# Kernel tuning notes

Measured on AMD Instinct MI355X. Metric: run time of the kernel, lower is better.

Reference implementation:

```python
import jax, jax.numpy as jnp
import numpy as np

B, C, V, K, COUT = 4, 64, 40962, 9, 64  # graph_level 6 -> 10*4^6+2 = 40962 vertices


def setup_inputs() -> dict:
    key = jax.random.key(0)
    k1, k2, k3, k4, k5 = jax.random.split(key, 5)
    return {
        "x": jax.random.normal(k1, (B, C, V), dtype=jnp.float32),
        "index": jax.random.randint(k2, (V, K), 0, V),  # per-vertex neighbor ids
        "itp_mat": jax.random.normal(k3, (V, K, K), dtype=jnp.float32) * 0.2,
        "conv_w": jax.random.normal(k4, (COUT, C, 1, K), dtype=jnp.float32) * 0.05,
        "conv_b": jax.random.normal(k5, (COUT,), dtype=jnp.float32) * 0.05,
    }


def reference(x, index, itp_mat, conv_w, conv_b):
    # x: [B, C, V]. Original: permute(2,0,1) -> [V,B,C]; gather neighbors -> [V,K,B,C];
    # select_index = arange(V) (stride=1, select_index=None), so selection is identity.
    g = jnp.transpose(x, (2, 0, 1))[index]          # [V, K, B, C] neighbor gather
    g = jnp.transpose(g, (2, 3, 0, 1))              # [B, C, V, K]
    # Interploate: batched per-vertex matmul [B,C,V,1,K] @ [V,K,K] -> [B,C,V,1,K]
    itp = jnp.einsum('bcvk,vkj->bcvj', g, itp_mat)  # [B, C, V, K]
    # Conv2d with kernel (1, K): contracts C and K per vertex -> [B, COUT, V]
    out = jnp.einsum('bcvj,ocj->bov', itp, conv_w[:, :, 0, :]) + conv_b[None, :, None]
    # sparse_reset: scatter into zeros at select_index = arange(V) -> identity
    return out
```

## Files before the change

### kernel.cpp

```cpp
#include <hip/hip_runtime.h>
#include <hip/hip_bf16.h>

#define VN 40962
#define NG 10241
#define LDA_B 1168
#define LDS_TOT 18688
#define XT_BYTES (VN * 512)

typedef float f32x4 __attribute__((ext_vector_type(4)));
typedef __bf16 bf16x8 __attribute__((ext_vector_type(8)));

__global__ __launch_bounds__(256) void k_transpose(const float* __restrict__ x,
                                                   __bf16* __restrict__ xt) {
    __shared__ __bf16 tile[64][65];
    const int v0 = blockIdx.x * 64;
    const int t0 = blockIdx.y * 64;
    const int lane = threadIdx.x & 63;
    const int sub = threadIdx.x >> 6;

#pragma unroll
    for (int r = 0; r < 16; ++r) {
        const int t = t0 + r * 4 + sub;
        const int v = v0 + lane;
        float val = (v < VN) ? x[(size_t)t * VN + v] : 0.f;
        tile[r * 4 + sub][lane] = (__bf16)val;
    }
    __syncthreads();
#pragma unroll
    for (int r = 0; r < 16; ++r) {
        const int vv = r * 4 + sub;
        const int v = v0 + vv;
        if (v < VN) xt[(size_t)v * 256 + t0 + lane] = tile[lane][vv];
    }
}

__global__ __launch_bounds__(64) void k_wprep(const float* __restrict__ conv_w,
                                              __bf16* __restrict__ wf) {
    const int id = blockIdx.x;
    const int ks = id % 18;
    const int w  = id / 18;
    const int lane = threadIdx.x;
    const int o  = w * 16 + (lane & 15);
    const int kb = (lane >> 4) * 8;
    const float* wrow = conv_w + (size_t)o * 576 + ks * 32 + kb;
    bf16x8 f;
#pragma unroll
    for (int e = 0; e < 8; ++e) f[e] = (__bf16)wrow[e];
    *(bf16x8*)(wf + ((size_t)id * 64 + lane) * 8) = f;
}

__global__ __launch_bounds__(256) void k_fused(const __bf16* __restrict__ xt,
                                               const int* __restrict__ index,
                                               const float* __restrict__ itp_mat,
                                               const __bf16* __restrict__ wf,
                                               const float* __restrict__ conv_b,
                                               float* __restrict__ out) {
    __shared__ char smem[LDS_TOT];

    const int tid  = threadIdx.x;
    const int lane = tid & 63;
    const int w    = tid >> 6;
    const int l16  = lane & 15;
    const int g4   = lane >> 4;

    int g;
    {
        const int bid = blockIdx.x;
        const int xcd = bid & 7;
        const int idx = bid >> 3;
        g = (xcd == 0) ? idx : (1281 + (xcd - 1) * 1280 + idx);
    }
    const int v0 = g * 4;

    float gv[4][9];
#pragma unroll
    for (int vv = 0; vv < 4; ++vv) {
        const int v  = v0 + vv;
        const int vm = (v < VN) ? v : VN - 1;
        const int* idxv = index + (size_t)vm * 9;
#pragma unroll
        for (int k = 0; k < 9; ++k)
            gv[vv][k] = (float)xt[(size_t)idxv[k] * 256 + tid];
    }
#pragma unroll
    for (int vv = 0; vv < 4; ++vv) {
        const int v  = v0 + vv;
        const int vm = (v < VN) ? v : VN - 1;
        const float* am = itp_mat + (size_t)vm * 81;
        float s[9];
#pragma unroll
        for (int j = 0; j < 9; ++j) s[j] = 0.f;
#pragma unroll
        for (int k = 0; k < 9; ++k) {
            const float gk = gv[vv][k];
#pragma unroll
            for (int j = 0; j < 9; ++j) s[j] += gk * am[k * 9 + j];
        }
        __bf16* rowp = (__bf16*)(smem + (vv * 4 + w) * LDA_B) + lane * 9;
#pragma unroll
        for (int j = 0; j < 9; ++j) rowp[j] = (__bf16)s[j];
    }
    __syncthreads();

    f32x4 acc = {0.f, 0.f, 0.f, 0.f};
    {
        const char* ar = smem + l16 * LDA_B + g4 * 16;
        const __bf16* wfp = wf + ((size_t)(w * 18) * 64 + lane) * 8;
#pragma unroll
        for (int ks = 0; ks < 18; ++ks) {
            bf16x8 a  = *(const bf16x8*)(ar + ks * 64);
            bf16x8 wb = *(const bf16x8*)(wfp + (size_t)ks * 512);
            acc = __builtin_amdgcn_mfma_f32_16x16x32_bf16(wb, a, acc, 0, 0, 0);
        }
    }

    {
        const int vvs = l16 >> 2;
        const int bs  = l16 & 3;
        const int v_s = v0 + vvs;
        const int o_b = w * 16 + g4 * 4;
        const f32x4 bias4 = *(const f32x4*)(conv_b + o_b);
        if (v_s < VN) {
            float* ob = out + (size_t)(bs * 64 + o_b) * VN + v_s;
#pragma unroll
            for (int r = 0; r < 4; ++r)
                ob[(size_t)r * VN] = acc[r] + bias4[r];
        }
    }
}

extern "C" void kernel_launch(void* const* d_in, const int* in_sizes, int n_in,
                              void* d_out, int out_size, void* d_ws, size_t ws_size,
                              hipStream_t stream) {
    const float* x       = (const float*)d_in[0];
    const int*   index   = (const int*)d_in[1];
    const float* itp_mat = (const float*)d_in[2];
    const float* conv_w  = (const float*)d_in[3];
    const float* conv_b  = (const float*)d_in[4];
    float* out = (float*)d_out;

    __bf16* xt = (__bf16*)d_ws;
    __bf16* wfrag = (__bf16*)((char*)d_ws + XT_BYTES);

    dim3 tgrid((VN + 63) / 64, 4, 1);
    k_transpose<<<tgrid, 256, 0, stream>>>(x, xt);
    k_wprep<<<72, 64, 0, stream>>>(conv_w, wfrag);
    k_fused<<<NG, 256, 0, stream>>>(xt, index, itp_mat, wfrag, conv_b, out);
}
```

Baseline: 86.82 us.

## Process two vertex groups per block and prefetch the second gather during MFMA

Each block now handles 8 vertices in two halves of 4, halving the grid. The gather for the second half is issued before the first half's MFMA and store, so its global load latency can overlap with compute. __syncthreads is replaced by a raw lgkmcnt wait plus s_barrier, which avoids waiting on outstanding vector memory loads. In exchange it uses more registers for the second gather buffer, which may lower occupancy, and it leaves fewer blocks in flight.

```diff
diff --git a/kernel.cpp b/kernel.cpp
--- a/kernel.cpp
+++ b/kernel.cpp
@@ -2,7 +2,7 @@
 #include <hip/hip_bf16.h>
 
 #define VN 40962
-#define NG 10241
+#define NGB 5121
 #define LDA_B 1168
 #define LDS_TOT 18688
 #define XT_BYTES (VN * 512)
@@ -68,65 +68,90 @@
         const int bid = blockIdx.x;
         const int xcd = bid & 7;
         const int idx = bid >> 3;
-        g = (xcd == 0) ? idx : (1281 + (xcd - 1) * 1280 + idx);
+        g = (xcd == 0) ? idx : (641 + (xcd - 1) * 640 + idx);
     }
-    const int v0 = g * 4;
+    const int v0 = g * 8;
+
+    const int vvs = l16 >> 2;
+    const int bs  = l16 & 3;
+    const int o_b = w * 16 + g4 * 4;
+    const f32x4 bias4 = *(const f32x4*)(conv_b + o_b);
+    float* const ob_base = out + (size_t)(bs * 64 + o_b) * VN;
+
+    const char* ar = smem + l16 * LDA_B + g4 * 16;
+    const __bf16* wfp = wf + ((size_t)(w * 18) * 64 + lane) * 8;
+
+#define INTERP_WRITE(GV, VBASE)                                               \
+    _Pragma("unroll")                                                         \
+    for (int vv = 0; vv < 4; ++vv) {                                          \
+        const int v  = (VBASE) + vv;                                          \
+        const int vm = (v < VN) ? v : VN - 1;                                 \
+        const float* am = itp_mat + (size_t)vm * 81;         \
+        float s[9];                                                           \
+        _Pragma("unroll")                                                     \
+        for (int j = 0; j < 9; ++j) s[j] = 0.f;                               \
+        _Pragma("unroll")                                                     \
+        for (int k = 0; k < 9; ++k) {                                         \
+            const float gk = GV[vv][k];                                       \
+            _Pragma("unroll")                                                 \
+            for (int j = 0; j < 9; ++j) s[j] += gk * am[k * 9 + j];           \
+        }                                                                     \
+        __bf16* rowp = (__bf16*)(smem + (vv * 4 + w) * LDA_B) + lane * 9;     \
+        _Pragma("unroll")                                                     \
+        for (int j = 0; j < 9; ++j) rowp[j] = (__bf16)s[j];                   \
+    }
+
+#define GATHER(GV, VBASE)                                                     \
+    _Pragma("unroll")                                                         \
+    for (int vv = 0; vv < 4; ++vv) {                                          \
+        const int v  = (VBASE) + vv;                                          \
+        const int vm = (v < VN) ? v : VN - 1;                                 \
+        const int* idxv = index + (size_t)vm * 9;                 \
+        _Pragma("unroll")                                                     \
+        for (int k = 0; k < 9; ++k)                                           \
+            GV[vv][k] = (float)xt[(size_t)idxv[k] * 256 + tid];               \
+    }
+
+#define MFMA_STORE(VBASE) {                                                   \
+    f32x4 acc = {0.f, 0.f, 0.f, 0.f};                                         \
+    _Pragma("unroll")                                                         \
+    for (int ks = 0; ks < 18; ++ks) {                                         \
+        bf16x8 a  = *(const bf16x8*)(ar + ks * 64);                           \
+        bf16x8 wb = *(const bf16x8*)(wfp + (size_t)ks * 512);                 \
+        acc = __builtin_amdgcn_mfma_f32_16x16x32_bf16(wb, a, acc, 0, 0, 0);   \
+    }                                                                         \
+    const int v_s = (VBASE) + vvs;                                            \
+    if (v_s < VN) {                                                           \
+        float* ob = ob_base + v_s;                                            \
+        _Pragma("unroll")                                                     \
+        for (int r = 0; r < 4; ++r)                                           \
+            ob[(size_t)r * VN] = acc[r] + bias4[r];                           \
+    } }
+
+#define RAW_BARRIER() do {                                                    \
+        asm volatile("s_waitcnt lgkmcnt(0)" ::: "memory");                    \
+        __builtin_amdgcn_s_barrier();                                         \
+    } while (0)
 
     float gv[4][9];
-#pragma unroll
-    for (int vv = 0; vv < 4; ++vv) {
-        const int v  = v0 + vv;
-        const int vm = (v < VN) ? v : VN - 1;
-        const int* idxv = index + (size_t)vm * 9;
-#pragma unroll
-        for (int k = 0; k < 9; ++k)
-            gv[vv][k] = (float)xt[(size_t)idxv[k] * 256 + tid];
-    }
-#pragma unroll
-    for (int vv = 0; vv < 4; ++vv) {
-        const int v  = v0 + vv;
-        const int vm = (v < VN) ? v : VN - 1;
-        const float* am = itp_mat + (size_t)vm * 81;
-        float s[9];
-#pragma unroll
-        for (int j = 0; j < 9; ++j) s[j] = 0.f;
-#pragma unroll
-        for (int k = 0; k < 9; ++k) {
-            const float gk = gv[vv][k];
-#pragma unroll
-            for (int j = 0; j < 9; ++j) s[j] += gk * am[k * 9 + j];
-        }
-        __bf16* rowp = (__bf16*)(smem + (vv * 4 + w) * LDA_B) + lane * 9;
-#pragma unroll
-        for (int j = 0; j < 9; ++j) rowp[j] = (__bf16)s[j];
-    }
-    __syncthreads();
+    GATHER(gv, v0)
+    INTERP_WRITE(gv, v0)
 
-    f32x4 acc = {0.f, 0.f, 0.f, 0.f};
-    {
-        const char* ar = smem + l16 * LDA_B + g4 * 16;
-        const __bf16* wfp = wf + ((size_t)(w * 18) * 64 + lane) * 8;
-#pragma unroll
-        for (int ks = 0; ks < 18; ++ks) {
-            bf16x8 a  = *(const bf16x8*)(ar + ks * 64);
-            bf16x8 wb = *(const bf16x8*)(wfp + (size_t)ks * 512);
-            acc = __builtin_amdgcn_mfma_f32_16x16x32_bf16(wb, a, acc, 0, 0, 0);
-        }
-    }
+    float gn[4][9];
+    GATHER(gn, v0 + 4)
 
-    {
-        const int vvs = l16 >> 2;
-        const int bs  = l16 & 3;
-        const int v_s = v0 + vvs;
-        const int o_b = w * 16 + g4 * 4;
-        const f32x4 bias4 = *(const f32x4*)(conv_b + o_b);
-        if (v_s < VN) {
-            float* ob = out + (size_t)(bs * 64 + o_b) * VN + v_s;
-#pragma unroll
-            for (int r = 0; r < 4; ++r)
-                ob[(size_t)r * VN] = acc[r] + bias4[r];
-        }
-    }
+    RAW_BARRIER();
+    MFMA_STORE(v0)
+    RAW_BARRIER();
+
+    INTERP_WRITE(gn, v0 + 4)
+    RAW_BARRIER();
+    MFMA_STORE(v0 + 4)
+
+#undef INTERP_WRITE
+#undef GATHER
+#undef MFMA_STORE
+#undef RAW_BARRIER
 }
 
 extern "C" void kernel_launch(void* const* d_in, const int* in_sizes, int n_in,
@@ -145,5 +170,5 @@
     dim3 tgrid((VN + 63) / 64, 4, 1);
     k_transpose<<<tgrid, 256, 0, stream>>>(x, xt);
     k_wprep<<<72, 64, 0, stream>>>(conv_w, wfrag);
-    k_fused<<<NG, 256, 0, stream>>>(xt, index, itp_mat, wfrag, conv_b, out);
+    k_fused<<<NGB, 256, 0, stream>>>(xt, index, itp_mat, wfrag, conv_b, out);
 }
```

After: 102.0 us. 1.17x slower.
